# Performance work log

Measured on AMD Instinct MI355X. Metric: run time of the kernel, lower is better.

## Reference

```python
import jax, jax.numpy as jnp
import numpy as np

B, S, H = 8, 160, 128
W_SIZE, V_SIZE, A_SIZE = 300, 35, 74


def setup_inputs() -> dict:
    key = jax.random.key(0)
    keys = iter(jax.random.split(key, 80))

    def rn(shape, scale=0.05):
        return jax.random.normal(next(keys), shape, dtype=jnp.float32) * scale

    inp = {}
    inp["w"] = rn((B, S, W_SIZE), 1.0)
    inp["v"] = rn((B, S, V_SIZE), 1.0)
    inp["a"] = rn((B, S, A_SIZE), 1.0)
    inp["lengths"] = jnp.full((B,), S, dtype=jnp.int32)  # full-length sequences

    def add_lstm(p, in_size, h_size):
        inp[p + "_Wih"] = rn((4 * h_size, in_size))
        inp[p + "_Whh"] = rn((4 * h_size, h_size))
        inp[p + "_bih"] = rn((4 * h_size,))
        inp[p + "_bhh"] = rn((4 * h_size,))

    add_lstm("w", W_SIZE, H)
    add_lstm("v", V_SIZE, H)
    add_lstm("a", A_SIZE, H)
    add_lstm("c", 3 * H, 3 * H)

    def add_xattn(p, h):
        inp[p + "_W1"] = rn((h, 2 * h))  # Linear(2h, h)
        inp[p + "_b1"] = rn((h,))
        inp[p + "_w2"] = rn((h,))        # Linear(h, 1, bias=False)

    add_xattn("vw", H)
    add_xattn("aw", H)
    add_xattn("sa", 3 * H)

    inp["mp_w"] = rn((H,))
    inp["mp_b"] = rn((1,))
    inp["fc1_W"] = rn((H, 5 * H))
    inp["fc1_b"] = rn((H,))
    inp["fc2_W"] = rn((1, H))
    inp["fc2_b"] = rn((1,))
    return inp


def lstm(x, Wih, Whh, bih, bhh):
    # single-layer batch_first LSTM, PyTorch gate order (i, f, g, o)
    b = x.shape[0]
    h = Whh.shape[1]
    xg = jnp.einsum('bsi,gi->bsg', x, Wih) + bih + bhh  # [B,S,4H]

    def step(carry, xt):
        hp, cp = carry
        g = xt + hp @ Whh.T
        i, f, gg, o = jnp.split(g, 4, axis=-1)
        c = jax.nn.sigmoid(f) * cp + jax.nn.sigmoid(i) * jnp.tanh(gg)
        hn = jax.nn.sigmoid(o) * jnp.tanh(c)
        return (hn, c), hn

    init = (jnp.zeros((b, h), x.dtype), jnp.zeros((b, h), x.dtype))
    _, hs = jax.lax.scan(step, init, jnp.swapaxes(xg, 0, 1))
    return jnp.swapaxes(hs, 0, 1)  # [B,S,H]


def cross_attention(src_hs, tgt_hs, mask, W1, b1, w2):
    # additive (Bahdanau) attention; attn_1(cat([src, tgt])) split into two GEMMs
    h = src_hs.shape[-1]
    s = src_hs @ W1[:, :h].T              # [B,V,Hd]
    t = tgt_hs @ W1[:, h:].T + b1         # [B,W,Hd]
    # [B,W,V,Hd] broadcast-add + tanh, then reduce with w2 -> scores [B,W,V]
    scores = jnp.einsum('bwvd,d->bwv', jnp.tanh(t[:, :, None, :] + s[:, None, :, :]), w2)
    scores = mask * scores                # multiplicative mask (as in original)
    weights = jax.nn.softmax(scores, axis=2)
    out = jnp.einsum('bwv,bvh->bwh', weights, src_hs)
    return out, weights


def soft_attention(reps, w, b):
    weights = jax.nn.softmax(reps @ w + b[0], axis=1)  # [B,S]
    out = jnp.einsum('bs,bsh->bh', weights, reps)
    return out, weights[:, :, None]


def reference(w, v, a, lengths,
              w_Wih, w_Whh, w_bih, w_bhh,
              v_Wih, v_Whh, v_bih, v_bhh,
              a_Wih, a_Whh, a_bih, a_bhh,
              c_Wih, c_Whh, c_bih, c_bhh,
              vw_W1, vw_b1, vw_w2,
              aw_W1, aw_b1, aw_w2,
              sa_W1, sa_b1, sa_w2,
              mp_w, mp_b, fc1_W, fc1_b, fc2_W, fc2_b):
    b, s = w.shape[0], w.shape[1]
    w_hs = lstm(w, w_Wih, w_Whh, w_bih, w_bhh)
    v_hs = lstm(v, v_Wih, v_Whh, v_bih, v_bhh)
    a_hs = lstm(a, a_Wih, a_Whh, a_bih, a_bhh)

    len_mask = (jnp.arange(s)[None, :] < lengths[:, None]).astype(w_hs.dtype)  # [B,S]
    mask3 = jnp.broadcast_to(len_mask[:, None, :], (b, s, s))                  # [B,W,V]

    v_out, v_attn_w = cross_attention(v_hs, w_hs, mask3, vw_W1, vw_b1, vw_w2)
    a_out, a_attn_w = cross_attention(a_hs, w_hs, mask3, aw_W1, aw_b1, aw_w2)

    c_hs = lstm(jnp.concatenate([w_hs, v_out, a_out], axis=2), c_Wih, c_Whh, c_bih, c_bhh)
    c_attn_out, _ = cross_attention(c_hs, c_hs, mask3, sa_W1, sa_b1, sa_w2)
    c_out = c_attn_out[jnp.arange(b), lengths - 1]  # last valid timestep, [B,3H]

    v_comp, v_soft_w = soft_attention(v_hs, mp_w, mp_b)
    a_comp, a_soft_w = soft_attention(a_hs, mp_w, mp_b)

    feat = jnp.concatenate([c_out, v_comp, a_comp], axis=-1)  # [B,5H]
    out = jax.nn.relu(feat @ fc1_W.T + fc1_b) @ fc2_W.T + fc2_b  # dropout = identity (eval)
    return out.reshape(-1), v_attn_w, v_soft_w, a_attn_w, a_soft_w
```

## Files before the change

kernel.cpp:

```cpp
#include <hip/hip_runtime.h>
#include <hip/hip_fp16.h>

typedef unsigned int u32;
typedef unsigned long long u64;

#define B 8
#define S 160
#define H 128
#define H3 384
#define G4 512
#define CG 1536
#define WIN 300
#define VIN 35
#define AIN 74

#define XG_W   0
#define XG_V   (XG_W + B*S*G4)
#define XG_A   (XG_V + B*S*G4)
#define HS_W   (XG_A + B*S*G4)
#define HS_V   (HS_W + B*S*H)
#define HS_A   (HS_V + B*S*H)
#define S_VW   (HS_A + B*S*H)
#define T_VW   (S_VW + B*S*H)
#define S_AW   (T_VW + B*S*H)
#define T_AW   (S_AW + B*S*H)
#define C_X    (T_AW + B*S*H)
#define S_SA   (C_X + B*S*H3)
#define WIHT_W (S_SA + B*S*H3)
#define WIHT_V (WIHT_W + WIN*G4)
#define WIHT_A (WIHT_V + VIN*G4)
#define WIHT_C (WIHT_A + AIN*G4)
#define WHHT_W (WIHT_C + H3*CG)
#define WHHT_V (WHHT_W + H*G4)
#define WHHT_A (WHHT_V + H*G4)
#define SAT_S  (WHHT_A + H*G4)
#define SAT_T  (SAT_S + H3*H3)
#define VW_ST  (SAT_T + H3*H3)
#define VW_TT  (VW_ST + H*H)
#define AW_ST  (VW_TT + H*H)
#define AW_TT  (AW_ST + H*H)
#define BSUM_W (AW_TT + H*H)
#define BSUM_V (BSUM_W + G4)
#define BSUM_A (BSUM_V + G4)
#define BSUM_C (BSUM_A + G4)
#define VCOMP  (BSUM_C + CG)
#define ACOMP  (VCOMP + B*H)
#define C_OUT  (ACOMP + B*H)
#define XGC16  (C_OUT + B*H3)
#define WRES   (XGC16 + B*S*CG/2)
#define CHS16  (WRES + CG*H3/2)
#define H_X    (CHS16 + B*S*H3/2)

#define O_VATT  8
#define O_VSOFT (8 + B*S*S)
#define O_AATT  (O_VSOFT + B*S)
#define O_ASOFT (O_AATT + B*S*S)

#define REP32(M) M(0)M(1)M(2)M(3)M(4)M(5)M(6)M(7)M(8)M(9)M(10)M(11)M(12)M(13)M(14)M(15)M(16)M(17)M(18)M(19)M(20)M(21)M(22)M(23)M(24)M(25)M(26)M(27)M(28)M(29)M(30)M(31)
#define REP48(M) REP32(M) M(32)M(33)M(34)M(35)M(36)M(37)M(38)M(39)M(40)M(41)M(42)M(43)M(44)M(45)M(46)M(47)

__device__ __forceinline__ float sigf(float x){ return 1.f/(1.f+__expf(-x)); }
__device__ __forceinline__ float tanhfast(float x){ float e=__expf(2.f*x); return 1.f - 2.f/(e+1.f); }
__device__ __forceinline__ float wred_sum(float x){
#pragma unroll
  for (int o=32;o;o>>=1) x += __shfl_xor(x,o);
  return x;
}
__device__ __forceinline__ float wred_max(float x){
#pragma unroll
  for (int o=32;o;o>>=1) x = fmaxf(x,__shfl_xor(x,o));
  return x;
}
__device__ __forceinline__ u32 packh2(float lo, float hi){
  __half a=__float2half_rn(lo), b=__float2half_rn(hi);
  return ((u32)__half_as_ushort(b)<<16) | (u32)__half_as_ushort(a);
}

typedef _Float16 h2v __attribute__((ext_vector_type(2)));
#if defined(__has_builtin)
#if __has_builtin(__builtin_amdgcn_fdot2)
#define HAVE_FDOT2 1
#endif
#endif
__device__ __forceinline__ float fdot2f(u32 w, u32 h, float acc){
#ifdef HAVE_FDOT2
  return __builtin_amdgcn_fdot2(__builtin_bit_cast(h2v,w), __builtin_bit_cast(h2v,h), acc, false);
#else
  h2v a=__builtin_bit_cast(h2v,w), b=__builtin_bit_cast(h2v,h);
  return acc + (float)a.x*(float)b.x + (float)a.y*(float)b.y;
#endif
}

#define PREP_TOT (3*G4 + CG + WIN*G4 + VIN*G4 + AIN*G4 + H3*CG + 3*H*G4 + 2*H3*H3 + 4*H*H + CG*H3/2)
__global__ void k0_prep(float* __restrict__ ws, u32* __restrict__ wsu,
    const float* __restrict__ wWih, const float* __restrict__ wWhh, const float* __restrict__ wbih, const float* __restrict__ wbhh,
    const float* __restrict__ vWih, const float* __restrict__ vWhh, const float* __restrict__ vbih, const float* __restrict__ vbhh,
    const float* __restrict__ aWih, const float* __restrict__ aWhh, const float* __restrict__ abih, const float* __restrict__ abhh,
    const float* __restrict__ cWih, const float* __restrict__ cWhh, const float* __restrict__ cbih, const float* __restrict__ cbhh,
    const float* __restrict__ vwW1, const float* __restrict__ awW1, const float* __restrict__ saW1)
{
  int idx = blockIdx.x*256 + threadIdx.x;
  if (idx >= PREP_TOT) return;
  if (idx < G4){ ws[BSUM_W+idx]=wbih[idx]+wbhh[idx]; return; } idx -= G4;
  if (idx < G4){ ws[BSUM_V+idx]=vbih[idx]+vbhh[idx]; return; } idx -= G4;
  if (idx < G4){ ws[BSUM_A+idx]=abih[idx]+abhh[idx]; return; } idx -= G4;
  if (idx < CG){ ws[BSUM_C+idx]=cbih[idx]+cbhh[idx]; return; } idx -= CG;
  if (idx < WIN*G4){ int k=idx/G4,g=idx%G4; ws[WIHT_W+idx]=wWih[g*WIN+k]; return; } idx -= WIN*G4;
  if (idx < VIN*G4){ int k=idx/G4,g=idx%G4; ws[WIHT_V+idx]=vWih[g*VIN+k]; return; } idx -= VIN*G4;
  if (idx < AIN*G4){ int k=idx/G4,g=idx%G4; ws[WIHT_A+idx]=aWih[g*AIN+k]; return; } idx -= AIN*G4;
  if (idx < H3*CG){ int k=idx/CG,g=idx%CG; ws[WIHT_C+idx]=cWih[g*H3+k]; return; } idx -= H3*CG;
  if (idx < H*G4){ int q=idx&3, r=idx>>2, g=r&511, k4=r>>9; ws[WHHT_W+idx]=wWhh[g*H + 4*k4+q]; return; } idx -= H*G4;
  if (idx < H*G4){ int q=idx&3, r=idx>>2, g=r&511, k4=r>>9; ws[WHHT_V+idx]=vWhh[g*H + 4*k4+q]; return; } idx -= H*G4;
  if (idx < H*G4){ int q=idx&3, r=idx>>2, g=r&511, k4=r>>9; ws[WHHT_A+idx]=aWhh[g*H + 4*k4+q]; return; } idx -= H*G4;
  if (idx < H3*H3){ int k=idx/H3,d=idx%H3; ws[SAT_S+idx]=saW1[d*(2*H3)+k]; return; } idx -= H3*H3;
  if (idx < H3*H3){ int k=idx/H3,d=idx%H3; ws[SAT_T+idx]=saW1[d*(2*H3)+H3+k]; return; } idx -= H3*H3;
  if (idx < H*H){ int k=idx/H,d=idx%H; ws[VW_ST+idx]=vwW1[d*(2*H)+k]; return; } idx -= H*H;
  if (idx < H*H){ int k=idx/H,d=idx%H; ws[VW_TT+idx]=vwW1[d*(2*H)+H+k]; return; } idx -= H*H;
  if (idx < H*H){ int k=idx/H,d=idx%H; ws[AW_ST+idx]=awW1[d*(2*H)+k]; return; } idx -= H*H;
  if (idx < H*H){ int k=idx/H,d=idx%H; ws[AW_TT+idx]=awW1[d*(2*H)+H+k]; return; } idx -= H*H;
  {
    int q = idx & 3; int r = idx >> 2;
    int ul = r & 127; int r2 = r >> 7;
    int k8 = r2 % 48; int jj = r2 / 48;
    int sl = jj >> 2, j = jj & 3;
    int gate = j*H3 + sl*128 + ul;
    int k2 = 4*k8 + q;
    wsu[WRES+idx] = packh2(cWhh[gate*H3 + 2*k2], cWhh[gate*H3 + 2*k2 + 1]);
  }
}

__global__ void k1_xg(float* __restrict__ ws,
    const float* __restrict__ xw, const float* __restrict__ xv, const float* __restrict__ xa)
{
  int bid = blockIdx.x;
  int lstm = bid/160; int rem = bid%160; int b = rem/20; int s0 = (rem%20)*8;
  int in_dim; const float* x; const float* wT; const float* bs; float* xg;
  if (lstm==0){ in_dim=WIN; x=xw; wT=ws+WIHT_W; bs=ws+BSUM_W; xg=ws+XG_W; }
  else if (lstm==1){ in_dim=VIN; x=xv; wT=ws+WIHT_V; bs=ws+BSUM_V; xg=ws+XG_V; }
  else { in_dim=AIN; x=xa; wT=ws+WIHT_A; bs=ws+BSUM_A; xg=ws+XG_A; }
  __shared__ float xt[8][WIN];
  int tid = threadIdx.x;
  for (int i=tid; i<8*in_dim; i+=256){ int r=i/in_dim, k=i%in_dim; xt[r][k] = x[((size_t)(b*S+s0+r))*in_dim + k]; }
  __syncthreads();
  float acc0[8], acc1[8];
  float b0 = bs[tid], b1 = bs[tid+256];
#pragma unroll
  for (int r=0;r<8;r++){ acc0[r]=b0; acc1[r]=b1; }
  for (int k=0;k<in_dim;k++){
    float w0 = wT[k*G4 + tid], w1 = wT[k*G4 + 256 + tid];
#pragma unroll
    for (int r=0;r<8;r++){ float xx = xt[r][k]; acc0[r] = fmaf(xx,w0,acc0[r]); acc1[r] = fmaf(xx,w1,acc1[r]); }
  }
#pragma unroll
  for (int r=0;r<8;r++){
    size_t ro = (size_t)(b*S+s0+r)*G4;
    xg[ro + tid] = acc0[r];
    xg[ro + 256 + tid] = acc1[r];
  }
}

__global__ __launch_bounds__(512,1) void k2_lstm(float* __restrict__ ws)
{
  int lstm = blockIdx.x >> 3, b = blockIdx.x & 7;
  const float* xg; const float* whhT; float* hs; float* cx = nullptr;
  if (lstm==0){ xg=ws+XG_W; whhT=ws+WHHT_W; hs=ws+HS_W; cx=ws+C_X; }
  else if (lstm==1){ xg=ws+XG_V; whhT=ws+WHHT_V; hs=ws+HS_V; }
  else { xg=ws+XG_A; whhT=ws+WHHT_A; hs=ws+HS_A; }
  int g = threadIdx.x;
  const float4* wb = ((const float4*)whhT) + g;
#define K2_LD(i) float4 w##i = wb[(i)*512];
  REP32(K2_LD)
  __shared__ __align__(16) float hbuf[H];
  __shared__ float gsum[G4];
  float c_reg = 0.f;
  if (g < H) hbuf[g] = 0.f;
  const float* xgb = xg + (size_t)b*S*G4;
  float* hsb = hs + (size_t)b*S*H;
  float* cxb = cx ? cx + (size_t)b*S*H3 : nullptr;
  float xg_cur = xgb[g];
  __syncthreads();
  const float4* h4p = (const float4*)hbuf;
  for (int t=0;t<S;t++){
    float acc = xg_cur;
    float xg_nxt = (t+1<S) ? xgb[(size_t)(t+1)*G4 + g] : 0.f;
#define K2_FMA(i) { float4 h4 = h4p[i]; acc = fmaf(w##i.x,h4.x,acc); acc = fmaf(w##i.y,h4.y,acc); acc = fmaf(w##i.z,h4.z,acc); acc = fmaf(w##i.w,h4.w,acc); }
    REP32(K2_FMA)
    gsum[g] = acc;
    xg_cur = xg_nxt;
    __syncthreads();
    if (g < H){
      float gi=gsum[g], gf=gsum[H+g], gg=gsum[2*H+g], go=gsum[3*H+g];
      c_reg = sigf(gf)*c_reg + sigf(gi)*tanhfast(gg);
      float h = sigf(go)*tanhfast(c_reg);
      hbuf[g] = h;
      hsb[(size_t)t*H + g] = h;
      if (cxb) cxb[(size_t)t*H3 + g] = h;
    }
    __syncthreads();
  }
}

__global__ void k3a_proj(float* __restrict__ ws, const float* __restrict__ vwb1, const float* __restrict__ awb1)
{
  int bid = blockIdx.x;
  int p = bid/160; int rem = bid%160; int b = rem/20; int s0 = (rem%20)*8;
  const float* src; const float* wT; const float* bias=nullptr; float* dst;
  if (p==0){ src=ws+HS_V; wT=ws+VW_ST; dst=ws+S_VW; }
  else if (p==1){ src=ws+HS_W; wT=ws+VW_TT; bias=vwb1; dst=ws+T_VW; }
  else if (p==2){ src=ws+HS_A; wT=ws+AW_ST; dst=ws+S_AW; }
  else { src=ws+HS_W; wT=ws+AW_TT; bias=awb1; dst=ws+T_AW; }
  __shared__ float xr[8][H];
  int tid = threadIdx.x;
  for (int i=tid;i<8*H;i+=128){ int r=i>>7, k=i&127; xr[r][k] = src[(size_t)(b*S+s0+r)*H + k]; }
  __syncthreads();
  float acc[8];
  float bv = bias ? bias[tid] : 0.f;
#pragma unroll
  for (int r=0;r<8;r++) acc[r]=bv;
  for (int k=0;k<H;k++){
    float wv = wT[k*H + tid];
#pragma unroll
    for (int r=0;r<8;r++) acc[r] = fmaf(xr[r][k], wv, acc[r]);
  }
#pragma unroll
  for (int r=0;r<8;r++) dst[(size_t)(b*S+s0+r)*H + tid] = acc[r];
}

__global__ void k3b_attn(float* __restrict__ ws, float* __restrict__ dout,
    const int* __restrict__ lengths, const float* __restrict__ vww2, const float* __restrict__ aww2)
{
  int wid = threadIdx.x >> 6, lane = threadIdx.x & 63;
  int row = blockIdx.x*4 + wid;
  int A = row / (B*S); int rem = row % (B*S); int b = rem / S; int w = rem % S;
  const float* sp = ws + (A? S_AW : S_VW) + (size_t)(b*S)*H;
  const float* tp = ws + (A? T_AW : T_VW) + (size_t)(b*S + w)*H;
  const float* w2 = A? aww2 : vww2;
  const float* src = ws + (A? HS_A : HS_V) + (size_t)(b*S)*H;
  float* attw = dout + (A? O_AATT : O_VATT) + (size_t)b*S*S + (size_t)w*S;
  int len = lengths[b];
  __shared__ float sc[4][S];
  float2 t2 = ((const float2*)tp)[lane];
  float2 w22 = ((const float2*)w2)[lane];
  for (int v=0; v<S; v++){
    float2 s2 = ((const float2*)(sp + (size_t)v*H))[lane];
    float x0 = tanhfast(t2.x + s2.x), x1 = tanhfast(t2.y + s2.y);
    float p = wred_sum(x0*w22.x + x1*w22.y);
    if (lane==0) sc[wid][v] = p;
  }
  __syncthreads();
  float m0 = (lane      < len)? sc[wid][lane]     : 0.f;
  float m1 = (lane+64   < len)? sc[wid][lane+64]  : 0.f;
  float m2 = (lane<32) ? ((lane+128 < len)? sc[wid][lane+128] : 0.f) : -1e30f;
  float m = wred_max(fmaxf(fmaxf(m0,m1),m2));
  float e0 = __expf(m0-m), e1 = __expf(m1-m), e2 = (lane<32)? __expf(m2-m) : 0.f;
  float inv = 1.f / wred_sum(e0+e1+e2);
  e0*=inv; e1*=inv; e2*=inv;
  sc[wid][lane] = e0; sc[wid][lane+64] = e1; if (lane<32) sc[wid][128+lane] = e2;
  attw[lane] = e0; attw[lane+64] = e1; if (lane<32) attw[128+lane] = e2;
  __syncthreads();
  float2 acc; acc.x=0.f; acc.y=0.f;
  for (int v=0; v<S; v++){
    float wg = sc[wid][v];
    float2 sv = ((const float2*)(src + (size_t)v*H))[lane];
    acc.x = fmaf(wg, sv.x, acc.x); acc.y = fmaf(wg, sv.y, acc.y);
  }
  float* cxr = ws + C_X + (size_t)(b*S + w)*H3 + (A? 2*H : H);
  ((float2*)cxr)[lane] = acc;
}

__global__ void k4_soft(float* __restrict__ ws, float* __restrict__ dout,
    const float* __restrict__ mpw, const float* __restrict__ mpb)
{
  int A = blockIdx.x >> 3, b = blockIdx.x & 7;
  const float* reps = ws + (A? HS_A : HS_V) + (size_t)(b*S)*H;
  float* softw = dout + (A? O_ASOFT : O_VSOFT) + b*S;
  float* comp = ws + (A? ACOMP : VCOMP) + b*H;
  __shared__ float sc[S]; __shared__ float wg[S];
  int wid = threadIdx.x >> 6, lane = threadIdx.x & 63;
  float bb = mpb[0];
  for (int s=wid; s<S; s+=4){
    float2 r2 = ((const float2*)(reps + (size_t)s*H))[lane];
    float2 m2 = ((const float2*)mpw)[lane];
    float p = wred_sum(r2.x*m2.x + r2.y*m2.y);
    if (lane==0) sc[s] = p + bb;
  }
  __syncthreads();
  if (threadIdx.x < 64){
    float m0 = sc[lane], m1 = sc[lane+64], m2 = (lane<32)? sc[lane+128] : -1e30f;
    float m = wred_max(fmaxf(fmaxf(m0,m1),m2));
    float e0=__expf(m0-m), e1=__expf(m1-m), e2=(lane<32)?__expf(m2-m):0.f;
    float inv = 1.f / wred_sum(e0+e1+e2);
    e0*=inv; e1*=inv; e2*=inv;
    wg[lane]=e0; wg[lane+64]=e1; if (lane<32) wg[128+lane]=e2;
    softw[lane]=e0; softw[lane+64]=e1; if (lane<32) softw[128+lane]=e2;
  }
  __syncthreads();
  if (threadIdx.x < H){
    float acc=0.f;
    for (int s=0;s<S;s++) acc = fmaf(wg[s], reps[(size_t)s*H + threadIdx.x], acc);
    comp[threadIdx.x] = acc;
  }
}

__global__ void k5_xgc(float* __restrict__ ws, u32* __restrict__ wsu)
{
  int b = blockIdx.x/40; int s0 = (blockIdx.x%40)*4;
  const float* cxb = ws + C_X + (size_t)(b*S+s0)*H3;
  const float* wT = ws + WIHT_C;
  const float* bs = ws + BSUM_C;
  __half* xgc = (__half*)(wsu + XGC16);
  __shared__ float xr[4][H3];
  int tid = threadIdx.x;
  for (int i=tid;i<4*H3;i+=512){ int r=i/H3, k=i%H3; xr[r][k]=cxb[(size_t)r*H3+k]; }
  __syncthreads();
  float acc[4][3];
  float b0=bs[tid], b1=bs[tid+512], b2=bs[tid+1024];
#pragma unroll
  for (int r=0;r<4;r++){ acc[r][0]=b0; acc[r][1]=b1; acc[r][2]=b2; }
  for (int k=0;k<H3;k++){
    float w0=wT[(size_t)k*CG+tid], w1=wT[(size_t)k*CG+512+tid], w2v=wT[(size_t)k*CG+1024+tid];
#pragma unroll
    for (int r=0;r<4;r++){
      float xx = xr[r][k];
      acc[r][0]=fmaf(xx,w0,acc[r][0]); acc[r][1]=fmaf(xx,w1,acc[r][1]); acc[r][2]=fmaf(xx,w2v,acc[r][2]);
    }
  }
#pragma unroll
  for (int r=0;r<4;r++){
    size_t ro = (size_t)(b*S+s0+r)*CG;
    xgc[ro+tid] = __float2half_rn(acc[r][0]);
    xgc[ro+512+tid] = __float2half_rn(acc[r][1]);
    xgc[ro+1024+tid] = __float2half_rn(acc[r][2]);
  }
}

__global__ __launch_bounds__(512,1) void k6_clstm(float* __restrict__ ws, u32* __restrict__ wsu)
{
  int b = blockIdx.x & 7, sl = blockIdx.x >> 3;
  int tid = threadIdx.x, j = tid>>7, ul = tid&127, lane = tid&63;
  int jj = sl*4 + j;
  const __half* xgc = (const __half*)(wsu + XGC16);
  u32* chsb = wsu + CHS16 + (size_t)b*S*(H3/2);
  u64* hxb = (u64*)(wsu + H_X) + (size_t)b*2*192;
  const uint4* wb = ((const uint4*)(wsu + WRES)) + (size_t)jj*48*128 + ul;
#define K6_LD(i) uint4 w##i = wb[(i)*128];
  REP48(K6_LD)
  __shared__ __align__(16) u32 h2[H3/2];
  __shared__ float gsum[G4];
  float c0 = 0.f, c1 = 0.f;
  if (tid < H3/2) h2[tid] = 0u;
  const __half* xgb = xgc + (size_t)b*S*CG;
  int gate = j*H3 + sl*128 + ul;
  float xg_cur = __half2float(xgb[gate]);
  __syncthreads();
  const uint4* h2q = (const uint4*)h2;
  for (int t=0;t<S;t++){
    float acc = xg_cur;
    float xg_nxt = (t+1<S) ? __half2float(xgb[(size_t)(t+1)*CG + gate]) : 0.f;
#define K6_FD(i) { uint4 hh = h2q[i]; acc = fdot2f(w##i.x,hh.x,acc); acc = fdot2f(w##i.y,hh.y,acc); acc = fdot2f(w##i.z,hh.z,acc); acc = fdot2f(w##i.w,hh.w,acc); }
    REP48(K6_FD)
    gsum[tid] = acc;
    xg_cur = xg_nxt;
    __syncthreads();
    int par = t & 1;
    u32 target = (u32)(t>>1) + 1u;
    if (tid < 64){
      int p0 = 2*lane, p1 = 2*lane+1;
      float gi0=gsum[p0], gf0=gsum[128+p0], gg0=gsum[256+p0], go0=gsum[384+p0];
      float gi1=gsum[p1], gf1=gsum[128+p1], gg1=gsum[256+p1], go1=gsum[384+p1];
      c0 = sigf(gf0)*c0 + sigf(gi0)*tanhfast(gg0);
      c1 = sigf(gf1)*c1 + sigf(gi1)*tanhfast(gg1);
      float h0 = sigf(go0)*tanhfast(c0);
      float h1 = sigf(go1)*tanhfast(c1);
      u32 pk = packh2(h0,h1);
      h2[sl*64 + lane] = pk;
      chsb[(size_t)t*(H3/2) + sl*64 + lane] = pk;
      __hip_atomic_store(&hxb[(size_t)par*192 + sl*64 + lane],
                         ((u64)target<<32) | (u64)pk,
                         __ATOMIC_RELAXED, __HIP_MEMORY_SCOPE_AGENT);
    } else if (tid >= 128 && tid < 256){
      int grp = (tid-128)>>6;
      int psl = sl + 1 + grp; if (psl >= 3) psl -= 3;
      u64* src = &hxb[(size_t)par*192 + psl*64 + lane];
      u64 v;
      do {
        v = __hip_atomic_load(src, __ATOMIC_RELAXED, __HIP_MEMORY_SCOPE_AGENT);
      } while ((u32)(v>>32) != target);
      h2[psl*64 + lane] = (u32)v;
    }
    __syncthreads();
  }
}

__global__ void k7a_sproj(float* __restrict__ ws, u32* __restrict__ wsu)
{
  int b = blockIdx.x/40; int v0 = (blockIdx.x%40)*4;
  const __half* chs = (const __half*)(wsu + CHS16);
  const float* wT = ws + SAT_S;
  __shared__ float xr[4][H3];
  int tid = threadIdx.x;
  for (int i=tid;i<4*H3;i+=384){ int r=i/H3, k=i%H3; xr[r][k] = __half2float(chs[(size_t)(b*S+v0+r)*H3 + k]); }
  __syncthreads();
  float acc[4] = {0.f,0.f,0.f,0.f};
  for (int k=0;k<H3;k++){
    float wv = wT[(size_t)k*H3 + tid];
#pragma unroll
    for (int r=0;r<4;r++) acc[r] = fmaf(xr[r][k], wv, acc[r]);
  }
#pragma unroll
  for (int r=0;r<4;r++) ws[S_SA + (size_t)(b*S+v0+r)*H3 + tid] = acc[r];
}

__global__ void k7b_sa(float* __restrict__ ws, u32* __restrict__ wsu,
    const int* __restrict__ lengths, const float* __restrict__ sab1, const float* __restrict__ saw2)
{
  int b = blockIdx.x;
  int len = lengths[b]; int tr = len-1;
  const __half* chs = (const __half*)(wsu + CHS16);
  __shared__ float tv[H3]; __shared__ float chr[H3]; __shared__ float sc[S]; __shared__ float wg[S];
  int tid = threadIdx.x, wid = tid>>6, lane = tid&63;
  chr[tid] = __half2float(chs[(size_t)(b*S+tr)*H3 + tid]);
  __syncthreads();
  float acc = sab1[tid];
  for (int k=0;k<H3;k++) acc = fmaf(chr[k], ws[SAT_T + (size_t)k*H3 + tid], acc);
  tv[tid] = acc;
  __syncthreads();
  for (int v=wid; v<S; v+=6){
    const float* sr = ws + S_SA + (size_t)(b*S+v)*H3;
    float p = 0.f;
#pragma unroll
    for (int q=0;q<6;q++){
      int d = lane + 64*q;
      p = fmaf(tanhfast(tv[d] + sr[d]), saw2[d], p);
    }
    p = wred_sum(p);
    if (lane==0) sc[v] = p;
  }
  __syncthreads();
  if (tid < 64){
    float m0 = (lane<len)? sc[lane]:0.f;
    float m1 = (lane+64<len)? sc[lane+64]:0.f;
    float m2 = (lane<32)? ((lane+128<len)? sc[lane+128]:0.f) : -1e30f;
    float m = wred_max(fmaxf(fmaxf(m0,m1),m2));
    float e0=__expf(m0-m), e1=__expf(m1-m), e2=(lane<32)?__expf(m2-m):0.f;
    float inv = 1.f / wred_sum(e0+e1+e2);
    wg[lane]=e0*inv; wg[lane+64]=e1*inv; if (lane<32) wg[128+lane]=e2*inv;
  }
  __syncthreads();
  float o = 0.f;
  for (int v=0; v<S; v++) o = fmaf(wg[v], __half2float(chs[(size_t)(b*S+v)*H3 + tid]), o);
  ws[C_OUT + (size_t)b*H3 + tid] = o;
}

__global__ void k8_mlp(float* __restrict__ ws, float* __restrict__ dout,
    const float* __restrict__ fc1W, const float* __restrict__ fc1b,
    const float* __restrict__ fc2W, const float* __restrict__ fc2b)
{
  int b = blockIdx.x, tid = threadIdx.x;
  __shared__ float feat[5*H]; __shared__ float r1[H];
  for (int i=tid;i<5*H;i+=128){
    float val;
    if (i < H3) val = ws[C_OUT + (size_t)b*H3 + i];
    else if (i < H3+H) val = ws[VCOMP + b*H + (i-H3)];
    else val = ws[ACOMP + b*H + (i-H3-H)];
    feat[i] = val;
  }
  __syncthreads();
  float acc = fc1b[tid];
  for (int k=0;k<5*H;k++) acc = fmaf(feat[k], fc1W[(size_t)tid*5*H + k], acc);
  r1[tid] = fmaxf(acc, 0.f) * fc2W[tid];
  __syncthreads();
  if (tid < 64){
    float p = r1[tid] + r1[tid+64];
    p = wred_sum(p);
    if (tid==0) dout[b] = p + fc2b[0];
  }
}

extern "C" void kernel_launch(void* const* d_in, const int* in_sizes, int n_in,
                              void* d_out, int out_size, void* d_ws, size_t ws_size,
                              hipStream_t stream) {
  const float* xw = (const float*)d_in[0];
  const float* xv = (const float*)d_in[1];
  const float* xa = (const float*)d_in[2];
  const int* lengths = (const int*)d_in[3];
  const float* wWih=(const float*)d_in[4], *wWhh=(const float*)d_in[5], *wbih=(const float*)d_in[6], *wbhh=(const float*)d_in[7];
  const float* vWih=(const float*)d_in[8], *vWhh=(const float*)d_in[9], *vbih=(const float*)d_in[10], *vbhh=(const float*)d_in[11];
  const float* aWih=(const float*)d_in[12], *aWhh=(const float*)d_in[13], *abih=(const float*)d_in[14], *abhh=(const float*)d_in[15];
  const float* cWih=(const float*)d_in[16], *cWhh=(const float*)d_in[17], *cbih=(const float*)d_in[18], *cbhh=(const float*)d_in[19];
  const float* vwW1=(const float*)d_in[20], *vwb1=(const float*)d_in[21], *vww2=(const float*)d_in[22];
  const float* awW1=(const float*)d_in[23], *awb1=(const float*)d_in[24], *aww2=(const float*)d_in[25];
  const float* saW1=(const float*)d_in[26], *sab1=(const float*)d_in[27], *saw2=(const float*)d_in[28];
  const float* mpw=(const float*)d_in[29], *mpb=(const float*)d_in[30];
  const float* fc1W=(const float*)d_in[31], *fc1b=(const float*)d_in[32];
  const float* fc2W=(const float*)d_in[33], *fc2b=(const float*)d_in[34];
  float* ws = (float*)d_ws;
  u32* wsu = (u32*)d_ws;
  float* dout = (float*)d_out;

  hipLaunchKernelGGL(k0_prep, dim3((PREP_TOT+255)/256), dim3(256), 0, stream,
      ws, wsu, wWih,wWhh,wbih,wbhh, vWih,vWhh,vbih,vbhh, aWih,aWhh,abih,abhh,
      cWih,cWhh,cbih,cbhh, vwW1, awW1, saW1);
  hipLaunchKernelGGL(k1_xg, dim3(480), dim3(256), 0, stream, ws, xw, xv, xa);
  hipLaunchKernelGGL(k2_lstm, dim3(24), dim3(512), 0, stream, ws);
  hipLaunchKernelGGL(k3a_proj, dim3(640), dim3(128), 0, stream, ws, vwb1, awb1);
  hipLaunchKernelGGL(k3b_attn, dim3(640), dim3(256), 0, stream, ws, dout, lengths, vww2, aww2);
  hipLaunchKernelGGL(k4_soft, dim3(16), dim3(256), 0, stream, ws, dout, mpw, mpb);
  hipLaunchKernelGGL(k5_xgc, dim3(B*40), dim3(512), 0, stream, ws, wsu);
  hipLaunchKernelGGL(k6_clstm, dim3(24), dim3(512), 0, stream, ws, wsu);
  hipLaunchKernelGGL(k7a_sproj, dim3(B*40), dim3(384), 0, stream, ws, wsu);
  hipLaunchKernelGGL(k7b_sa, dim3(B), dim3(384), 0, stream, ws, wsu, lengths, sab1, saw2);
  hipLaunchKernelGGL(k8_mlp, dim3(B), dim3(128), 0, stream, ws, dout, fc1W, fc1b, fc2W, fc2b);
}
```

Baseline: 980.6 us.

## Repartition LSTM recurrences: split-K in small LSTMs, batch-shared weights in c-LSTM

The three small LSTM kernels now use 1024 threads with two threads per gate row, each holding half of Whh in registers read straight from the input. A shuffle combines the two partial sums, so the transposed-Whh prep step goes away. The combined LSTM kernel is repartitioned across 24 blocks by hidden-unit slices covering all 8 batch rows. Each block keeps only a small weight slice and reduces over 8 K-slices with shuffles, with xgc stored batch-interleaved. Every block must now exchange its full hidden state through global atomic slots each step, so spin traffic and synchronisation cost grow.

```diff
diff --git a/kernel.cpp b/kernel.cpp
--- a/kernel.cpp
+++ b/kernel.cpp
@@ -30,10 +30,7 @@
 #define WIHT_V (WIHT_W + WIN*G4)
 #define WIHT_A (WIHT_V + VIN*G4)
 #define WIHT_C (WIHT_A + AIN*G4)
-#define WHHT_W (WIHT_C + H3*CG)
-#define WHHT_V (WHHT_W + H*G4)
-#define WHHT_A (WHHT_V + H*G4)
-#define SAT_S  (WHHT_A + H*G4)
+#define SAT_S  (WIHT_C + H3*CG)
 #define SAT_T  (SAT_S + H3*H3)
 #define VW_ST  (SAT_T + H3*H3)
 #define VW_TT  (VW_ST + H*H)
@@ -56,8 +53,7 @@
 #define O_AATT  (O_VSOFT + B*S)
 #define O_ASOFT (O_AATT + B*S*S)
 
-#define REP32(M) M(0)M(1)M(2)M(3)M(4)M(5)M(6)M(7)M(8)M(9)M(10)M(11)M(12)M(13)M(14)M(15)M(16)M(17)M(18)M(19)M(20)M(21)M(22)M(23)M(24)M(25)M(26)M(27)M(28)M(29)M(30)M(31)
-#define REP48(M) REP32(M) M(32)M(33)M(34)M(35)M(36)M(37)M(38)M(39)M(40)M(41)M(42)M(43)M(44)M(45)M(46)M(47)
+#define REP16(M) M(0)M(1)M(2)M(3)M(4)M(5)M(6)M(7)M(8)M(9)M(10)M(11)M(12)M(13)M(14)M(15)
 
 __device__ __forceinline__ float sigf(float x){ return 1.f/(1.f+__expf(-x)); }
 __device__ __forceinline__ float tanhfast(float x){ float e=__expf(2.f*x); return 1.f - 2.f/(e+1.f); }
@@ -91,11 +87,11 @@
 #endif
 }
 
-#define PREP_TOT (3*G4 + CG + WIN*G4 + VIN*G4 + AIN*G4 + H3*CG + 3*H*G4 + 2*H3*H3 + 4*H*H + CG*H3/2)
+#define PREP_TOT (3*G4 + CG + WIN*G4 + VIN*G4 + AIN*G4 + H3*CG + 2*H3*H3 + 4*H*H + CG*H3/2)
 __global__ void k0_prep(float* __restrict__ ws, u32* __restrict__ wsu,
-    const float* __restrict__ wWih, const float* __restrict__ wWhh, const float* __restrict__ wbih, const float* __restrict__ wbhh,
-    const float* __restrict__ vWih, const float* __restrict__ vWhh, const float* __restrict__ vbih, const float* __restrict__ vbhh,
-    const float* __restrict__ aWih, const float* __restrict__ aWhh, const float* __restrict__ abih, const float* __restrict__ abhh,
+    const float* __restrict__ wWih, const float* __restrict__ wbih, const float* __restrict__ wbhh,
+    const float* __restrict__ vWih, const float* __restrict__ vbih, const float* __restrict__ vbhh,
+    const float* __restrict__ aWih, const float* __restrict__ abih, const float* __restrict__ abhh,
     const float* __restrict__ cWih, const float* __restrict__ cWhh, const float* __restrict__ cbih, const float* __restrict__ cbhh,
     const float* __restrict__ vwW1, const float* __restrict__ awW1, const float* __restrict__ saW1)
 {
@@ -109,9 +105,6 @@
   if (idx < VIN*G4){ int k=idx/G4,g=idx%G4; ws[WIHT_V+idx]=vWih[g*VIN+k]; return; } idx -= VIN*G4;
   if (idx < AIN*G4){ int k=idx/G4,g=idx%G4; ws[WIHT_A+idx]=aWih[g*AIN+k]; return; } idx -= AIN*G4;
   if (idx < H3*CG){ int k=idx/CG,g=idx%CG; ws[WIHT_C+idx]=cWih[g*H3+k]; return; } idx -= H3*CG;
-  if (idx < H*G4){ int q=idx&3, r=idx>>2, g=r&511, k4=r>>9; ws[WHHT_W+idx]=wWhh[g*H + 4*k4+q]; return; } idx -= H*G4;
-  if (idx < H*G4){ int q=idx&3, r=idx>>2, g=r&511, k4=r>>9; ws[WHHT_V+idx]=vWhh[g*H + 4*k4+q]; return; } idx -= H*G4;
-  if (idx < H*G4){ int q=idx&3, r=idx>>2, g=r&511, k4=r>>9; ws[WHHT_A+idx]=aWhh[g*H + 4*k4+q]; return; } idx -= H*G4;
   if (idx < H3*H3){ int k=idx/H3,d=idx%H3; ws[SAT_S+idx]=saW1[d*(2*H3)+k]; return; } idx -= H3*H3;
   if (idx < H3*H3){ int k=idx/H3,d=idx%H3; ws[SAT_T+idx]=saW1[d*(2*H3)+H3+k]; return; } idx -= H3*H3;
   if (idx < H*H){ int k=idx/H,d=idx%H; ws[VW_ST+idx]=vwW1[d*(2*H)+k]; return; } idx -= H*H;
@@ -119,13 +112,12 @@
   if (idx < H*H){ int k=idx/H,d=idx%H; ws[AW_ST+idx]=awW1[d*(2*H)+k]; return; } idx -= H*H;
   if (idx < H*H){ int k=idx/H,d=idx%H; ws[AW_TT+idx]=awW1[d*(2*H)+H+k]; return; } idx -= H*H;
   {
-    int q = idx & 3; int r = idx >> 2;
-    int ul = r & 127; int r2 = r >> 7;
-    int k8 = r2 % 48; int jj = r2 / 48;
-    int sl = jj >> 2, j = jj & 3;
-    int gate = j*H3 + sl*128 + ul;
-    int k2 = 4*k8 + q;
-    wsu[WRES+idx] = packh2(cWhh[gate*H3 + 2*k2], cWhh[gate*H3 + 2*k2 + 1]);
+    int j = idx % 24; int th = idx / 24;
+    int s = th & 7; int r = (th >> 3) & 63; int p = th >> 9;
+    int g3 = r >> 4, m = r & 15;
+    int grow = g3*H3 + p*16 + m;
+    int k2 = s*24 + j;
+    wsu[WRES+idx] = packh2(cWhh[(size_t)grow*H3 + 2*k2], cWhh[(size_t)grow*H3 + 2*k2 + 1]);
   }
 }
 
@@ -159,43 +151,46 @@
   }
 }
 
-__global__ __launch_bounds__(512,1) void k2_lstm(float* __restrict__ ws)
+__global__ __launch_bounds__(1024) void k2_lstm(float* __restrict__ ws,
+    const float* __restrict__ wWhh, const float* __restrict__ vWhh, const float* __restrict__ aWhh)
 {
   int lstm = blockIdx.x >> 3, b = blockIdx.x & 7;
-  const float* xg; const float* whhT; float* hs; float* cx = nullptr;
-  if (lstm==0){ xg=ws+XG_W; whhT=ws+WHHT_W; hs=ws+HS_W; cx=ws+C_X; }
-  else if (lstm==1){ xg=ws+XG_V; whhT=ws+WHHT_V; hs=ws+HS_V; }
-  else { xg=ws+XG_A; whhT=ws+WHHT_A; hs=ws+HS_A; }
-  int g = threadIdx.x;
-  const float4* wb = ((const float4*)whhT) + g;
-#define K2_LD(i) float4 w##i = wb[(i)*512];
-  REP32(K2_LD)
+  const float* xg; const float* whh; float* hs; float* cx = nullptr;
+  if (lstm==0){ xg=ws+XG_W; whh=wWhh; hs=ws+HS_W; cx=ws+C_X; }
+  else if (lstm==1){ xg=ws+XG_V; whh=vWhh; hs=ws+HS_V; }
+  else { xg=ws+XG_A; whh=aWhh; hs=ws+HS_A; }
+  int tid = threadIdx.x;
+  int row = tid >> 1, s = tid & 1;
+  const float4* wb = (const float4*)(whh + (size_t)row*H + s*64);
+#define K2_LD(i) float4 w##i = wb[i];
+  REP16(K2_LD)
   __shared__ __align__(16) float hbuf[H];
   __shared__ float gsum[G4];
   float c_reg = 0.f;
-  if (g < H) hbuf[g] = 0.f;
+  if (tid < H) hbuf[tid] = 0.f;
   const float* xgb = xg + (size_t)b*S*G4;
   float* hsb = hs + (size_t)b*S*H;
   float* cxb = cx ? cx + (size_t)b*S*H3 : nullptr;
-  float xg_cur = xgb[g];
-  __syncthreads();
-  const float4* h4p = (const float4*)hbuf;
+  float xg_cur = xgb[row];
+  __syncthreads();
+  const float4* h4p = (const float4*)(hbuf + s*64);
   for (int t=0;t<S;t++){
-    float acc = xg_cur;
-    float xg_nxt = (t+1<S) ? xgb[(size_t)(t+1)*G4 + g] : 0.f;
+    float acc = 0.f;
 #define K2_FMA(i) { float4 h4 = h4p[i]; acc = fmaf(w##i.x,h4.x,acc); acc = fmaf(w##i.y,h4.y,acc); acc = fmaf(w##i.z,h4.z,acc); acc = fmaf(w##i.w,h4.w,acc); }
-    REP32(K2_FMA)
-    gsum[g] = acc;
-    xg_cur = xg_nxt;
+    REP16(K2_FMA)
+    acc += __shfl_xor(acc, 1);
+    float xg_nxt = (t+1<S) ? xgb[(size_t)(t+1)*G4 + row] : 0.f;
+    if (s == 0) gsum[row] = acc + xg_cur;
     __syncthreads();
-    if (g < H){
-      float gi=gsum[g], gf=gsum[H+g], gg=gsum[2*H+g], go=gsum[3*H+g];
+    if (tid < H){
+      float gi=gsum[tid], gf=gsum[H+tid], gg=gsum[2*H+tid], go=gsum[3*H+tid];
       c_reg = sigf(gf)*c_reg + sigf(gi)*tanhfast(gg);
       float h = sigf(go)*tanhfast(c_reg);
-      hbuf[g] = h;
-      hsb[(size_t)t*H + g] = h;
-      if (cxb) cxb[(size_t)t*H3 + g] = h;
+      hbuf[tid] = h;
+      hsb[(size_t)t*H + tid] = h;
+      if (cxb) cxb[(size_t)t*H3 + tid] = h;
     }
+    xg_cur = xg_nxt;
     __syncthreads();
   }
 }
@@ -327,67 +322,90 @@
   }
 #pragma unroll
   for (int r=0;r<4;r++){
-    size_t ro = (size_t)(b*S+s0+r)*CG;
-    xgc[ro+tid] = __float2half_rn(acc[r][0]);
-    xgc[ro+512+tid] = __float2half_rn(acc[r][1]);
-    xgc[ro+1024+tid] = __float2half_rn(acc[r][2]);
-  }
-}
-
-__global__ __launch_bounds__(512,1) void k6_clstm(float* __restrict__ ws, u32* __restrict__ wsu)
-{
-  int b = blockIdx.x & 7, sl = blockIdx.x >> 3;
-  int tid = threadIdx.x, j = tid>>7, ul = tid&127, lane = tid&63;
-  int jj = sl*4 + j;
+#pragma unroll
+    for (int part=0;part<3;part++){
+      int gate = part*512 + tid;
+      xgc[((size_t)(s0+r)*CG + gate)*8 + b] = __float2half_rn(acc[r][part]);
+    }
+  }
+}
+
+__global__ __launch_bounds__(512) void k6_clstm(float* __restrict__ ws, u32* __restrict__ wsu)
+{
+  int p = blockIdx.x;
+  int tid = threadIdx.x;
+  int r = tid >> 3, s = tid & 7, s6 = s*6;
+  int g3 = r >> 4, m = r & 15;
+  int grow = g3*H3 + p*16 + m;
   const __half* xgc = (const __half*)(wsu + XGC16);
-  u32* chsb = wsu + CHS16 + (size_t)b*S*(H3/2);
-  u64* hxb = (u64*)(wsu + H_X) + (size_t)b*2*192;
-  const uint4* wb = ((const uint4*)(wsu + WRES)) + (size_t)jj*48*128 + ul;
-#define K6_LD(i) uint4 w##i = wb[(i)*128];
-  REP48(K6_LD)
-  __shared__ __align__(16) u32 h2[H3/2];
-  __shared__ float gsum[G4];
-  float c0 = 0.f, c1 = 0.f;
-  if (tid < H3/2) h2[tid] = 0u;
-  const __half* xgb = xgc + (size_t)b*S*CG;
-  int gate = j*H3 + sl*128 + ul;
-  float xg_cur = __half2float(xgb[gate]);
+  u32* chs = wsu + CHS16;
+  u64* slots = (u64*)(wsu + H_X);
+  const uint4* wb = ((const uint4*)(wsu + WRES)) + ((size_t)(p*64 + r)*8 + s)*6;
+  uint4 w0=wb[0], w1=wb[1], w2=wb[2], w3=wb[3], w4=wb[4], w5=wb[5];
+  __shared__ __align__(16) u32 h2[8*192];
+  __shared__ float gsum[64*9];
+  float c_reg = 0.f;
+  for (int i=tid;i<8*192;i+=512) h2[i]=0u;
+  float xg_cur = __half2float(xgc[(size_t)grow*8 + s]);
   __syncthreads();
   const uint4* h2q = (const uint4*)h2;
+  int s0b = s&1, s1b = s&2, s2b = s&4;
   for (int t=0;t<S;t++){
-    float acc = xg_cur;
-    float xg_nxt = (t+1<S) ? __half2float(xgb[(size_t)(t+1)*CG + gate]) : 0.f;
-#define K6_FD(i) { uint4 hh = h2q[i]; acc = fdot2f(w##i.x,hh.x,acc); acc = fdot2f(w##i.y,hh.y,acc); acc = fdot2f(w##i.z,hh.z,acc); acc = fdot2f(w##i.w,hh.w,acc); }
-    REP48(K6_FD)
-    gsum[tid] = acc;
-    xg_cur = xg_nxt;
+#define K6_DOT(bi, dst) { const uint4* hb = h2q + (bi)*48 + s6; \
+    uint4 x0=hb[0],x1=hb[1],x2=hb[2],x3=hb[3],x4=hb[4],x5=hb[5]; \
+    float aA=0.f,aB=0.f; \
+    aA=fdot2f(w0.x,x0.x,aA); aB=fdot2f(w0.y,x0.y,aB); aA=fdot2f(w0.z,x0.z,aA); aB=fdot2f(w0.w,x0.w,aB); \
+    aA=fdot2f(w1.x,x1.x,aA); aB=fdot2f(w1.y,x1.y,aB); aA=fdot2f(w1.z,x1.z,aA); aB=fdot2f(w1.w,x1.w,aB); \
+    aA=fdot2f(w2.x,x2.x,aA); aB=fdot2f(w2.y,x2.y,aB); aA=fdot2f(w2.z,x2.z,aA); aB=fdot2f(w2.w,x2.w,aB); \
+    aA=fdot2f(w3.x,x3.x,aA); aB=fdot2f(w3.y,x3.y,aB); aA=fdot2f(w3.z,x3.z,aA); aB=fdot2f(w3.w,x3.w,aB); \
+    aA=fdot2f(w4.x,x4.x,aA); aB=fdot2f(w4.y,x4.y,aB); aA=fdot2f(w4.z,x4.z,aA); aB=fdot2f(w4.w,x4.w,aB); \
+    aA=fdot2f(w5.x,x5.x,aA); aB=fdot2f(w5.y,x5.y,aB); aA=fdot2f(w5.z,x5.z,aA); aB=fdot2f(w5.w,x5.w,aB); \
+    dst = aA + aB; }
+    float acc0,acc1,acc2,acc3,acc4,acc5,acc6,acc7;
+    K6_DOT(0,acc0) K6_DOT(1,acc1) K6_DOT(2,acc2) K6_DOT(3,acc3)
+    K6_DOT(4,acc4) K6_DOT(5,acc5) K6_DOT(6,acc6) K6_DOT(7,acc7)
+    float k0v = s0b? acc1:acc0, k0s = s0b? acc0:acc1;
+    float k1v = s0b? acc3:acc2, k1s = s0b? acc2:acc3;
+    float k2v = s0b? acc5:acc4, k2s = s0b? acc4:acc5;
+    float k3v = s0b? acc7:acc6, k3s = s0b? acc6:acc7;
+    k0v += __shfl_xor(k0s,1); k1v += __shfl_xor(k1s,1);
+    k2v += __shfl_xor(k2s,1); k3v += __shfl_xor(k3s,1);
+    float m0v = s1b? k1v:k0v, m0s = s1b? k0v:k1v;
+    float m1v = s1b? k3v:k2v, m1s = s1b? k2v:k3v;
+    m0v += __shfl_xor(m0s,2); m1v += __shfl_xor(m1s,2);
+    float f0 = s2b? m1v:m0v, f0s = s2b? m0v:m1v;
+    f0 += __shfl_xor(f0s,4);
+    float xg_nxt = (t+1<S)? __half2float(xgc[((size_t)(t+1)*CG + grow)*8 + s]) : 0.f;
+    gsum[r*9+s] = f0 + xg_cur;
     __syncthreads();
     int par = t & 1;
     u32 target = (u32)(t>>1) + 1u;
-    if (tid < 64){
-      int p0 = 2*lane, p1 = 2*lane+1;
-      float gi0=gsum[p0], gf0=gsum[128+p0], gg0=gsum[256+p0], go0=gsum[384+p0];
-      float gi1=gsum[p1], gf1=gsum[128+p1], gg1=gsum[256+p1], go1=gsum[384+p1];
-      c0 = sigf(gf0)*c0 + sigf(gi0)*tanhfast(gg0);
-      c1 = sigf(gf1)*c1 + sigf(gi1)*tanhfast(gg1);
-      float h0 = sigf(go0)*tanhfast(c0);
-      float h1 = sigf(go1)*tanhfast(c1);
-      u32 pk = packh2(h0,h1);
-      h2[sl*64 + lane] = pk;
-      chsb[(size_t)t*(H3/2) + sl*64 + lane] = pk;
-      __hip_atomic_store(&hxb[(size_t)par*192 + sl*64 + lane],
-                         ((u64)target<<32) | (u64)pk,
-                         __ATOMIC_RELAXED, __HIP_MEMORY_SCOPE_AGENT);
-    } else if (tid >= 128 && tid < 256){
-      int grp = (tid-128)>>6;
-      int psl = sl + 1 + grp; if (psl >= 3) psl -= 3;
-      u64* src = &hxb[(size_t)par*192 + psl*64 + lane];
-      u64 v;
-      do {
-        v = __hip_atomic_load(src, __ATOMIC_RELAXED, __HIP_MEMORY_SCOPE_AGENT);
-      } while ((u32)(v>>32) != target);
-      h2[psl*64 + lane] = (u32)v;
+    if (tid < 128){
+      int b = tid >> 4, mm = tid & 15;
+      float gi=gsum[mm*9+b], gf=gsum[(16+mm)*9+b], gg=gsum[(32+mm)*9+b], go=gsum[(48+mm)*9+b];
+      c_reg = sigf(gf)*c_reg + sigf(gi)*tanhfast(gg);
+      float h = sigf(go)*tanhfast(c_reg);
+      float h1 = __shfl_down(h, 1);
+      if (!(mm & 1)){
+        u32 pk = packh2(h, h1);
+        int k = p*8 + (mm>>1);
+        chs[((size_t)b*S + t)*192 + k] = pk;
+        if (t+1 < S)
+          __hip_atomic_store(&slots[(size_t)par*1536 + b*192 + k], ((u64)target<<32)|(u64)pk,
+                             __ATOMIC_RELAXED, __HIP_MEMORY_SCOPE_AGENT);
+      }
+    } else if (t+1 < S){
+      int base = (tid-128)*4;
+#pragma unroll
+      for (int q=0;q<4;q++){
+        int i = base + q;
+        u64 v;
+        do { v = __hip_atomic_load(&slots[(size_t)par*1536 + i], __ATOMIC_RELAXED, __HIP_MEMORY_SCOPE_AGENT); }
+        while ((u32)(v>>32) != target);
+        h2[i] = (u32)v;
+      }
     }
+    xg_cur = xg_nxt;
     __syncthreads();
   }
 }
@@ -499,10 +517,10 @@
   float* dout = (float*)d_out;
 
   hipLaunchKernelGGL(k0_prep, dim3((PREP_TOT+255)/256), dim3(256), 0, stream,
-      ws, wsu, wWih,wWhh,wbih,wbhh, vWih,vWhh,vbih,vbhh, aWih,aWhh,abih,abhh,
+      ws, wsu, wWih,wbih,wbhh, vWih,vbih,vbhh, aWih,abih,abhh,
       cWih,cWhh,cbih,cbhh, vwW1, awW1, saW1);
   hipLaunchKernelGGL(k1_xg, dim3(480), dim3(256), 0, stream, ws, xw, xv, xa);
-  hipLaunchKernelGGL(k2_lstm, dim3(24), dim3(512), 0, stream, ws);
+  hipLaunchKernelGGL(k2_lstm, dim3(24), dim3(1024), 0, stream, ws, wWhh, vWhh, aWhh);
   hipLaunchKernelGGL(k3a_proj, dim3(640), dim3(128), 0, stream, ws, vwb1, awb1);
   hipLaunchKernelGGL(k3b_attn, dim3(640), dim3(256), 0, stream, ws, dout, lengths, vww2, aww2);
   hipLaunchKernelGGL(k4_soft, dim3(16), dim3(256), 0, stream, ws, dout, mpw, mpb);
```

Result: slower. 1.231 ms (+25.6%).

## Split combined LSTM recurrence across six blocks per batch instead of three

Applied to the files above, without the earlier changes.

The recurrent combined LSTM kernel now splits the 384 hidden units of each batch across 6 blocks of 256 threads, each owning 64 units, instead of 3 blocks of 512 threads owning 128 units. The recurrent weight layout is re-packed to match. Each thread computes one gate and the hidden pairs are packed with a shuffle. Five groups of 32 threads poll the other slices' published halves through global atomics. The aim is to halve the per-block serial dot-product work each step and spread the recurrence over more compute units. The cost is more cross-block synchronisation traffic and polling per timestep.

```diff
diff --git a/kernel.cpp b/kernel.cpp
--- a/kernel.cpp
+++ b/kernel.cpp
@@ -120,12 +120,12 @@
   if (idx < H*H){ int k=idx/H,d=idx%H; ws[AW_TT+idx]=awW1[d*(2*H)+H+k]; return; } idx -= H*H;
   {
     int q = idx & 3; int r = idx >> 2;
-    int ul = r & 127; int r2 = r >> 7;
-    int k8 = r2 % 48; int jj = r2 / 48;
-    int sl = jj >> 2, j = jj & 3;
-    int gate = j*H3 + sl*128 + ul;
-    int k2 = 4*k8 + q;
-    wsu[WRES+idx] = packh2(cWhh[gate*H3 + 2*k2], cWhh[gate*H3 + 2*k2 + 1]);
+    int t = r & 255; int r2 = r >> 8;
+    int i = r2 % 48; int sl = r2 / 48;
+    int j = t >> 6, ul = t & 63;
+    int row = j*H3 + sl*64 + ul;
+    int k2 = i*4 + q;
+    wsu[WRES+idx] = packh2(cWhh[(size_t)row*H3 + 2*k2], cWhh[(size_t)row*H3 + 2*k2 + 1]);
   }
 }
 
@@ -327,66 +327,67 @@
   }
 #pragma unroll
   for (int r=0;r<4;r++){
-    size_t ro = (size_t)(b*S+s0+r)*CG;
-    xgc[ro+tid] = __float2half_rn(acc[r][0]);
-    xgc[ro+512+tid] = __float2half_rn(acc[r][1]);
-    xgc[ro+1024+tid] = __float2half_rn(acc[r][2]);
-  }
-}
-
-__global__ __launch_bounds__(512,1) void k6_clstm(float* __restrict__ ws, u32* __restrict__ wsu)
+    size_t ro = (size_t)(b*S + s0+r)*CG;
+    xgc[ro + tid]        = __float2half_rn(acc[r][0]);
+    xgc[ro + 512 + tid]  = __float2half_rn(acc[r][1]);
+    xgc[ro + 1024 + tid] = __float2half_rn(acc[r][2]);
+  }
+}
+
+__global__ __launch_bounds__(256,1) void k6_clstm(float* __restrict__ ws, u32* __restrict__ wsu)
 {
   int b = blockIdx.x & 7, sl = blockIdx.x >> 3;
-  int tid = threadIdx.x, j = tid>>7, ul = tid&127, lane = tid&63;
-  int jj = sl*4 + j;
-  const __half* xgc = (const __half*)(wsu + XGC16);
+  int tid = threadIdx.x, j = tid>>6, ul = tid&63;
+  const __half* xgb = ((const __half*)(wsu + XGC16)) + (size_t)b*S*CG;
   u32* chsb = wsu + CHS16 + (size_t)b*S*(H3/2);
-  u64* hxb = (u64*)(wsu + H_X) + (size_t)b*2*192;
-  const uint4* wb = ((const uint4*)(wsu + WRES)) + (size_t)jj*48*128 + ul;
-#define K6_LD(i) uint4 w##i = wb[(i)*128];
+  u64* slots = (u64*)(wsu + H_X);
+  const uint4* wb = ((const uint4*)(wsu + WRES)) + (size_t)sl*48*256 + tid;
+#define K6_LD(i) uint4 w##i = wb[(i)*256];
   REP48(K6_LD)
   __shared__ __align__(16) u32 h2[H3/2];
-  __shared__ float gsum[G4];
-  float c0 = 0.f, c1 = 0.f;
+  __shared__ float gsum[256];
+  float c_reg = 0.f;
   if (tid < H3/2) h2[tid] = 0u;
-  const __half* xgb = xgc + (size_t)b*S*CG;
-  int gate = j*H3 + sl*128 + ul;
-  float xg_cur = __half2float(xgb[gate]);
+  int row = j*H3 + sl*64 + ul;
+  float xg_cur = __half2float(xgb[row]);
   __syncthreads();
   const uint4* h2q = (const uint4*)h2;
   for (int t=0;t<S;t++){
     float acc = xg_cur;
-    float xg_nxt = (t+1<S) ? __half2float(xgb[(size_t)(t+1)*CG + gate]) : 0.f;
 #define K6_FD(i) { uint4 hh = h2q[i]; acc = fdot2f(w##i.x,hh.x,acc); acc = fdot2f(w##i.y,hh.y,acc); acc = fdot2f(w##i.z,hh.z,acc); acc = fdot2f(w##i.w,hh.w,acc); }
     REP48(K6_FD)
+    float xg_nxt = (t+1<S)? __half2float(xgb[(size_t)(t+1)*CG + row]) : 0.f;
     gsum[tid] = acc;
     xg_cur = xg_nxt;
     __syncthreads();
     int par = t & 1;
     u32 target = (u32)(t>>1) + 1u;
+    u64* sb = slots + ((size_t)par*8 + b)*192;
     if (tid < 64){
-      int p0 = 2*lane, p1 = 2*lane+1;
-      float gi0=gsum[p0], gf0=gsum[128+p0], gg0=gsum[256+p0], go0=gsum[384+p0];
-      float gi1=gsum[p1], gf1=gsum[128+p1], gg1=gsum[256+p1], go1=gsum[384+p1];
-      c0 = sigf(gf0)*c0 + sigf(gi0)*tanhfast(gg0);
-      c1 = sigf(gf1)*c1 + sigf(gi1)*tanhfast(gg1);
-      float h0 = sigf(go0)*tanhfast(c0);
-      float h1 = sigf(go1)*tanhfast(c1);
-      u32 pk = packh2(h0,h1);
-      h2[sl*64 + lane] = pk;
-      chsb[(size_t)t*(H3/2) + sl*64 + lane] = pk;
-      __hip_atomic_store(&hxb[(size_t)par*192 + sl*64 + lane],
-                         ((u64)target<<32) | (u64)pk,
-                         __ATOMIC_RELAXED, __HIP_MEMORY_SCOPE_AGENT);
-    } else if (tid >= 128 && tid < 256){
-      int grp = (tid-128)>>6;
-      int psl = sl + 1 + grp; if (psl >= 3) psl -= 3;
-      u64* src = &hxb[(size_t)par*192 + psl*64 + lane];
-      u64 v;
-      do {
-        v = __hip_atomic_load(src, __ATOMIC_RELAXED, __HIP_MEMORY_SCOPE_AGENT);
-      } while ((u32)(v>>32) != target);
-      h2[psl*64 + lane] = (u32)v;
+      float gi=gsum[tid], gf=gsum[64+tid], gg=gsum[128+tid], go=gsum[192+tid];
+      c_reg = sigf(gf)*c_reg + sigf(gi)*tanhfast(gg);
+      float h = sigf(go)*tanhfast(c_reg);
+      float h1 = __shfl_down(h, 1);
+      if (!(tid & 1)){
+        u32 pk = packh2(h, h1);
+        int p = sl*32 + (tid>>1);
+        h2[p] = pk;
+        chsb[(size_t)t*(H3/2) + p] = pk;
+        if (t+1 < S)
+          __hip_atomic_store(&sb[p], ((u64)target<<32) | (u64)pk,
+                             __ATOMIC_RELAXED, __HIP_MEMORY_SCOPE_AGENT);
+      }
+    } else if (t+1 < S){
+      int i = tid - 64;
+      if (i < 160){
+        int pi = i >> 5;
+        int psl = sl + 1 + pi; if (psl >= 6) psl -= 6;
+        int p = psl*32 + (i & 31);
+        u64 v;
+        do { v = __hip_atomic_load(&sb[p], __ATOMIC_RELAXED, __HIP_MEMORY_SCOPE_AGENT); }
+        while ((u32)(v>>32) != target);
+        h2[p] = (u32)v;
+      }
     }
     __syncthreads();
   }
@@ -507,7 +508,7 @@
   hipLaunchKernelGGL(k3b_attn, dim3(640), dim3(256), 0, stream, ws, dout, lengths, vww2, aww2);
   hipLaunchKernelGGL(k4_soft, dim3(16), dim3(256), 0, stream, ws, dout, mpw, mpb);
   hipLaunchKernelGGL(k5_xgc, dim3(B*40), dim3(512), 0, stream, ws, wsu);
-  hipLaunchKernelGGL(k6_clstm, dim3(24), dim3(512), 0, stream, ws, wsu);
+  hipLaunchKernelGGL(k6_clstm, dim3(48), dim3(256), 0, stream, ws, wsu);
   hipLaunchKernelGGL(k7a_sproj, dim3(B*40), dim3(384), 0, stream, ws, wsu);
   hipLaunchKernelGGL(k7b_sa, dim3(B), dim3(384), 0, stream, ws, wsu, lengths, sab1, saw2);
   hipLaunchKernelGGL(k8_mlp, dim3(B), dim3(128), 0, stream, ws, dout, fc1W, fc1b, fc2W, fc2b);
```

Result: faster. 958.4 us (-2.3%).
